# Optimization experiments

Hardware: AMD Instinct MI355X
Metric: run time of the kernel (lower is better)

The kernel has to match this reference:

```python
import jax, jax.numpy as jnp
import numpy as np

ALPHA = 1.0  # self.a buffer (alpha=1.0 default)


def setup_inputs() -> dict:
    key = jax.random.key(0)
    k1, k2, k3 = jax.random.split(key, 3)
    B, S, DIN, DOUT = 4, 2048, 4096, 4096
    # activations and weights are int8 in [-127, 127)
    x = jax.random.randint(k1, (B, S, DIN), -127, 127, dtype=jnp.int8)
    weight = jax.random.randint(k2, (DOUT, DIN), -127, 127, dtype=jnp.int8)
    bias = jax.random.normal(k3, (1, DOUT), dtype=jnp.float32)
    return {"x": x, "weight": weight, "bias": bias}


def reference(x, weight, bias):
    # x: [B, S, DIN] int8; weight: [DOUT, DIN] int8; bias: [1, DOUT] fp32
    x_shape = x.shape
    x2 = x.reshape(-1, x_shape[-1])  # [B*S, DIN]
    y = jnp.matmul(x2, weight.T, preferred_element_type=jnp.int32)  # [B*S, DOUT] int32
    # epilogue: y + round(bias / alpha); int32 + fp32 promotes to fp32 (matches torch)
    y = y.astype(jnp.float32) + jnp.round(bias / ALPHA)
    return y.reshape(*x_shape[:-1], y.shape[-1])
```

## Files before the change

kernel.cpp:

```cpp
#include <hip/hip_runtime.h>
#include <stdint.h>
#include <math.h>


typedef int i32x4 __attribute__((ext_vector_type(4)));

static constexpr int Mdim = 8192;
static constexpr int Ndim = 4096;
static constexpr int Kdim = 4096;
static constexpr int BM = 256;
static constexpr int BN = 256;
static constexpr int BKb = 128;
static constexpr int NKT = Kdim / BKb;
static constexpr int BUF_BYTES = 65536;

typedef const __attribute__((address_space(1))) unsigned int gu32;
typedef __attribute__((address_space(3))) unsigned int lu32;

__device__ __forceinline__ void gload_lds16(const int8_t* g, char* l) {
    __builtin_amdgcn_global_load_lds((gu32*)g, (lu32*)l, 16, 0, 0);
}

__global__ void pack_i32_to_i8(const int* __restrict__ in,
                               unsigned int* __restrict__ out, int n4) {
    int idx = blockIdx.x * blockDim.x + threadIdx.x;
    int stride = gridDim.x * blockDim.x;
    for (int i = idx; i < n4; i += stride) {
        i32x4 v = ((const i32x4*)in)[i];
        unsigned int o = ((unsigned)v[0] & 0xffu)
                       | (((unsigned)v[1] & 0xffu) << 8)
                       | (((unsigned)v[2] & 0xffu) << 16)
                       | (((unsigned)v[3]) << 24);
        out[i] = o;
    }
}

__global__ __launch_bounds__(512, 2) void w8a8_gemm_256(
    const int8_t* __restrict__ X, const int8_t* __restrict__ Wt,
    const float* __restrict__ bias, float* __restrict__ out)
{
    __shared__ char smem[2 * BUF_BYTES];

    const int tid = threadIdx.x;
    const int w   = tid >> 6;
    const int l   = tid & 63;
    const int fr  = l & 15;
    const int fk  = l >> 4;
    const int wm  = w >> 2;
    const int wn  = w & 3;

    const int bm = blockIdx.x * BM;
    const int bn = blockIdx.y * BN;

    const int8_t* gA = X  + (size_t)(bm + l) * Kdim + w * 16;
    const int8_t* gB = Wt + (size_t)(bn + l) * Kdim + w * 16;
    const int ldsAw = w * 2048 + l * 16;
    const int ldsBw = 32768 + w * 2048 + l * 16;

    auto stageA = [&](int t, int hm) {
        const int bufo = (t & 1) * BUF_BYTES;
        const size_t ko = (size_t)t * BKb;
#pragma unroll
        for (int s = 0; s < 2; ++s)
            gload_lds16(gA + (size_t)(hm * 128 + s * 64) * Kdim + ko,
                        &smem[bufo + hm * 16384 + s * 1024 + ldsAw]);
    };
    auto stageB = [&](int t, int hn) {
        const int bufo = (t & 1) * BUF_BYTES;
        const size_t ko = (size_t)t * BKb;
#pragma unroll
        for (int s = 0; s < 2; ++s)
            gload_lds16(gB + (size_t)(hn * 128 + s * 64) * Kdim + ko,
                        &smem[bufo + hn * 16384 + s * 1024 + ldsBw]);
    };

    const int aBase = wm * 16384 + fk * 2048 + fr * 16;
    const int bBase = 32768 + (wn >> 1) * 16384 + fk * 2048
                    + ((wn & 1) * 64 + fr) * 16;

    i32x4 acc[8][4] = {};
    i32x4 a[4][2], b[4][2];

    stageB(0, 0); stageB(0, 1); stageA(0, 0); stageA(0, 1);
    stageB(1, 0); stageB(1, 1);
    asm volatile("s_waitcnt vmcnt(4)" ::: "memory");
    __syncthreads();

    for (int t = 0; t < NKT; ++t) {
        const int p = (t & 1) * BUF_BYTES;

#pragma unroll
        for (int ks = 0; ks < 2; ++ks) {
#pragma unroll
            for (int j = 0; j < 4; ++j)
                a[j][ks] = *(const i32x4*)&smem[p + aBase + ks * 8192 + j * 256];
#pragma unroll
            for (int ni = 0; ni < 2; ++ni)
                b[ni][ks] = *(const i32x4*)&smem[p + bBase + ks * 8192 + ni * 256];
        }
        if (t + 1 < NKT) stageA(t + 1, 0);
        __builtin_amdgcn_s_barrier();
        asm volatile("s_waitcnt lgkmcnt(0)" ::: "memory");
        __builtin_amdgcn_sched_barrier(0);
        __builtin_amdgcn_s_setprio(1);
#pragma unroll
        for (int ks = 0; ks < 2; ++ks)
#pragma unroll
            for (int j = 0; j < 4; ++j)
#pragma unroll
                for (int ni = 0; ni < 2; ++ni)
                    acc[j][ni] = __builtin_amdgcn_mfma_i32_16x16x64_i8(
                        a[j][ks], b[ni][ks], acc[j][ni], 0, 0, 0);
        __builtin_amdgcn_s_setprio(0);
        __builtin_amdgcn_s_barrier();

#pragma unroll
        for (int ks = 0; ks < 2; ++ks)
#pragma unroll
            for (int ni = 2; ni < 4; ++ni)
                b[ni][ks] = *(const i32x4*)&smem[p + bBase + ks * 8192 + ni * 256];
        if (t + 1 < NKT) stageA(t + 1, 1);
        __builtin_amdgcn_s_barrier();
        asm volatile("s_waitcnt lgkmcnt(0)" ::: "memory");
        __builtin_amdgcn_sched_barrier(0);
        __builtin_amdgcn_s_setprio(1);
#pragma unroll
        for (int ks = 0; ks < 2; ++ks)
#pragma unroll
            for (int j = 0; j < 4; ++j)
#pragma unroll
                for (int ni = 2; ni < 4; ++ni)
                    acc[j][ni] = __builtin_amdgcn_mfma_i32_16x16x64_i8(
                        a[j][ks], b[ni][ks], acc[j][ni], 0, 0, 0);
        __builtin_amdgcn_s_setprio(0);
        __builtin_amdgcn_s_barrier();

#pragma unroll
        for (int ks = 0; ks < 2; ++ks)
#pragma unroll
            for (int j = 0; j < 4; ++j)
                a[j][ks] = *(const i32x4*)&smem[p + aBase + ks * 8192 + 1024 + j * 256];
        if (t + 2 < NKT) stageB(t + 2, 0);
        __builtin_amdgcn_s_barrier();
        asm volatile("s_waitcnt lgkmcnt(0)" ::: "memory");
        __builtin_amdgcn_sched_barrier(0);
        __builtin_amdgcn_s_setprio(1);
#pragma unroll
        for (int ks = 0; ks < 2; ++ks)
#pragma unroll
            for (int j = 0; j < 4; ++j)
#pragma unroll
                for (int ni = 0; ni < 2; ++ni)
                    acc[4 + j][ni] = __builtin_amdgcn_mfma_i32_16x16x64_i8(
                        a[j][ks], b[ni][ks], acc[4 + j][ni], 0, 0, 0);
        __builtin_amdgcn_s_setprio(0);
        __builtin_amdgcn_s_barrier();

        if (t + 2 < NKT) stageB(t + 2, 1);
        __builtin_amdgcn_s_barrier();
        __builtin_amdgcn_s_setprio(1);
#pragma unroll
        for (int ks = 0; ks < 2; ++ks)
#pragma unroll
            for (int j = 0; j < 4; ++j)
#pragma unroll
                for (int ni = 2; ni < 4; ++ni)
                    acc[4 + j][ni] = __builtin_amdgcn_mfma_i32_16x16x64_i8(
                        a[j][ks], b[ni][ks], acc[4 + j][ni], 0, 0, 0);
        __builtin_amdgcn_s_setprio(0);
        if (t + 1 < NKT) {
            if (t + 1 == NKT - 1) asm volatile("s_waitcnt vmcnt(0)" ::: "memory");
            else                  asm volatile("s_waitcnt vmcnt(4)" ::: "memory");
        }
        __builtin_amdgcn_s_barrier();
    }

    float bv[4];
#pragma unroll
    for (int ni = 0; ni < 4; ++ni)
        bv[ni] = rintf(bias[bn + wn * 64 + ni * 16 + fr]);
#pragma unroll
    for (int mi = 0; mi < 8; ++mi) {
        const int rbase = bm + wm * 128 + mi * 16 + fk * 4;
#pragma unroll
        for (int ni = 0; ni < 4; ++ni) {
            const int col = bn + wn * 64 + ni * 16 + fr;
#pragma unroll
            for (int r = 0; r < 4; ++r)
                out[(size_t)(rbase + r) * Ndim + col] = (float)acc[mi][ni][r] + bv[ni];
        }
    }
}

extern "C" void kernel_launch(void* const* d_in, const int* in_sizes, int n_in,
                              void* d_out, int out_size, void* d_ws, size_t ws_size,
                              hipStream_t stream) {
    const int*   X32  = (const int*)d_in[0];
    const int*   W32  = (const int*)d_in[1];
    const float* bias = (const float*)d_in[2];
    float* out = (float*)d_out;

    int8_t* Xp = (int8_t*)d_ws;
    int8_t* Wp = (int8_t*)d_ws + (size_t)Mdim * Kdim;

    const int nX4 = Mdim * Kdim / 4;
    const int nW4 = Ndim * Kdim / 4;
    pack_i32_to_i8<<<2048, 256, 0, stream>>>(X32, (unsigned int*)Xp, nX4);
    pack_i32_to_i8<<<2048, 256, 0, stream>>>(W32, (unsigned int*)Wp, nW4);

    dim3 grid(Mdim / BM, Ndim / BN);
    w8a8_gemm_256<<<grid, dim3(512), 0, stream>>>(Xp, Wp, bias, out);
}
```

Before: 411.6 us.

## Prefetch A and B two K-tiles ahead and merge the two pack kernels

The GEMM main loop now issues loads for both the A and B tiles of step t+2, rather than A at t+1 and B at t+2. Each tile is staged as soon as its double-buffer half has been fully read into registers, and one barrier per iteration is dropped. The vmcnt waits are adjusted to match the new number of loads in flight. The two int32-to-int8 pack launches are also merged into a single kernel that covers both tensors, which removes one launch. The extra loads in flight raise memory pressure, and correctness now depends on the new wait counts and barrier placement.

New measurement: 432.9 us. 5.2% more time.

```diff
diff --git a/kernel.cpp b/kernel.cpp
--- a/kernel.cpp
+++ b/kernel.cpp
@@ -21,17 +21,23 @@
     __builtin_amdgcn_global_load_lds((gu32*)g, (lu32*)l, 16, 0, 0);
 }
 
-__global__ void pack_i32_to_i8(const int* __restrict__ in,
-                               unsigned int* __restrict__ out, int n4) {
+__global__ void pack_i32_to_i8_both(const int* __restrict__ X32,
+                                    const int* __restrict__ W32,
+                                    unsigned int* __restrict__ Xp,
+                                    unsigned int* __restrict__ Wp,
+                                    int nX4, int nT4) {
     int idx = blockIdx.x * blockDim.x + threadIdx.x;
     int stride = gridDim.x * blockDim.x;
-    for (int i = idx; i < n4; i += stride) {
-        i32x4 v = ((const i32x4*)in)[i];
+    for (int i = idx; i < nT4; i += stride) {
+        const int* src; unsigned int* dst; int j;
+        if (i < nX4) { src = X32; dst = Xp; j = i; }
+        else         { src = W32; dst = Wp; j = i - nX4; }
+        i32x4 v = ((const i32x4*)src)[j];
         unsigned int o = ((unsigned)v[0] & 0xffu)
                        | (((unsigned)v[1] & 0xffu) << 8)
                        | (((unsigned)v[2] & 0xffu) << 16)
                        | (((unsigned)v[3]) << 24);
-        out[i] = o;
+        dst[j] = o;
     }
 }
 
@@ -82,8 +88,8 @@
     i32x4 a[4][2], b[4][2];
 
     stageB(0, 0); stageB(0, 1); stageA(0, 0); stageA(0, 1);
-    stageB(1, 0); stageB(1, 1);
-    asm volatile("s_waitcnt vmcnt(4)" ::: "memory");
+    stageB(1, 0); stageB(1, 1); stageA(1, 0); stageA(1, 1);
+    asm volatile("s_waitcnt vmcnt(8)" ::: "memory");
     __syncthreads();
 
     for (int t = 0; t < NKT; ++t) {
@@ -98,7 +104,6 @@
             for (int ni = 0; ni < 2; ++ni)
                 b[ni][ks] = *(const i32x4*)&smem[p + bBase + ks * 8192 + ni * 256];
         }
-        if (t + 1 < NKT) stageA(t + 1, 0);
         __builtin_amdgcn_s_barrier();
         asm volatile("s_waitcnt lgkmcnt(0)" ::: "memory");
         __builtin_amdgcn_sched_barrier(0);
@@ -119,7 +124,6 @@
 #pragma unroll
             for (int ni = 2; ni < 4; ++ni)
                 b[ni][ks] = *(const i32x4*)&smem[p + bBase + ks * 8192 + ni * 256];
-        if (t + 1 < NKT) stageA(t + 1, 1);
         __builtin_amdgcn_s_barrier();
         asm volatile("s_waitcnt lgkmcnt(0)" ::: "memory");
         __builtin_amdgcn_sched_barrier(0);
@@ -140,7 +144,7 @@
 #pragma unroll
             for (int j = 0; j < 4; ++j)
                 a[j][ks] = *(const i32x4*)&smem[p + aBase + ks * 8192 + 1024 + j * 256];
-        if (t + 2 < NKT) stageB(t + 2, 0);
+        if (t + 2 < NKT) { stageB(t + 2, 0); stageB(t + 2, 1); }
         __builtin_amdgcn_s_barrier();
         asm volatile("s_waitcnt lgkmcnt(0)" ::: "memory");
         __builtin_amdgcn_sched_barrier(0);
@@ -156,8 +160,8 @@
         __builtin_amdgcn_s_setprio(0);
         __builtin_amdgcn_s_barrier();
 
-        if (t + 2 < NKT) stageB(t + 2, 1);
-        __builtin_amdgcn_s_barrier();
+        if (t + 2 < NKT) { stageA(t + 2, 0); stageA(t + 2, 1); }
+        __builtin_amdgcn_sched_barrier(0);
         __builtin_amdgcn_s_setprio(1);
 #pragma unroll
         for (int ks = 0; ks < 2; ++ks)
@@ -168,10 +172,8 @@
                     acc[4 + j][ni] = __builtin_amdgcn_mfma_i32_16x16x64_i8(
                         a[j][ks], b[ni][ks], acc[4 + j][ni], 0, 0, 0);
         __builtin_amdgcn_s_setprio(0);
-        if (t + 1 < NKT) {
-            if (t + 1 == NKT - 1) asm volatile("s_waitcnt vmcnt(0)" ::: "memory");
-            else                  asm volatile("s_waitcnt vmcnt(4)" ::: "memory");
-        }
+        if (t + 2 < NKT)      asm volatile("s_waitcnt vmcnt(8)" ::: "memory");
+        else if (t + 1 < NKT) asm volatile("s_waitcnt vmcnt(0)" ::: "memory");
         __builtin_amdgcn_s_barrier();
     }
 
@@ -205,8 +207,8 @@
 
     const int nX4 = Mdim * Kdim / 4;
     const int nW4 = Ndim * Kdim / 4;
-    pack_i32_to_i8<<<2048, 256, 0, stream>>>(X32, (unsigned int*)Xp, nX4);
-    pack_i32_to_i8<<<2048, 256, 0, stream>>>(W32, (unsigned int*)Wp, nW4);
+    pack_i32_to_i8_both<<<4096, 256, 0, stream>>>(
+        X32, W32, (unsigned int*)Xp, (unsigned int*)Wp, nX4, nX4 + nW4);
 
     dim3 grid(Mdim / BM, Ndim / BN);
     w8a8_gemm_256<<<grid, dim3(512), 0, stream>>>(Xp, Wp, bias, out);
```
